# Optimization experiments

Hardware: AMD Instinct MI355X
Metric: run time of the kernel (lower is better)

The kernel has to match this reference:

```python
import jax, jax.numpy as jnp
import numpy as np

N_NODES = 50000
N_EDGES = 800000
IN_DIM = 256
OUT_DIM = 256


def setup_inputs() -> dict:
    key = jax.random.key(0)
    k_feat, k_src, k_dst, k_w0, k_w1, k_b = jax.random.split(key, 6)
    feat = jax.random.normal(k_feat, (N_NODES, IN_DIM), dtype=jnp.float32)
    src = jax.random.randint(k_src, (N_EDGES,), 0, N_NODES, dtype=jnp.int64)
    dst = jax.random.randint(k_dst, (N_EDGES,), 0, N_NODES, dtype=jnp.int64)
    # GraphConv weights (Glorot-ish scale) and biases
    W0 = jax.random.normal(k_w0, (IN_DIM, OUT_DIM), dtype=jnp.float32) / np.sqrt(IN_DIM)
    W1 = jax.random.normal(k_w1, (OUT_DIM, OUT_DIM), dtype=jnp.float32) / np.sqrt(OUT_DIM)
    b0 = jnp.zeros((OUT_DIM,), dtype=jnp.float32)
    b1 = jnp.zeros((OUT_DIM,), dtype=jnp.float32)
    # single shared nn.PReLU parameter (torch default init 0.25)
    prelu_a = jnp.asarray(0.25, dtype=jnp.float32)
    return {"feat": feat, "src": src, "dst": dst,
            "W0": W0, "b0": b0, "W1": W1, "b1": b1, "prelu_a": prelu_a}


def _prelu(x, a):
    return jnp.where(x >= 0, x, a * x)


def reference(feat, src, dst, W0, b0, W1, b1, prelu_a):
    N = feat.shape[0]
    ones = jnp.ones((src.shape[0],), dtype=feat.dtype)
    out_deg = jnp.zeros((N,), dtype=feat.dtype).at[src].add(ones)
    in_deg = jnp.zeros((N,), dtype=feat.dtype).at[dst].add(ones)
    # DGL norm='both': clamp degrees to >=1 before rsqrt
    norm_s = jax.lax.rsqrt(jnp.maximum(out_deg, 1.0))[:, None]  # [N,1]
    norm_d = jax.lax.rsqrt(jnp.maximum(in_deg, 1.0))[:, None]   # [N,1]

    def graph_conv(h, W, b):
        # h' = D_in^{-1/2} A (D_out^{-1/2} h) W + b
        msg = (h * norm_s)[src]                                   # [E, d]
        agg = jax.ops.segment_sum(msg, dst, num_segments=N)       # [N, d]
        return (agg * norm_d) @ W + b

    h = _prelu(graph_conv(feat, W0, b0), prelu_a)
    hg = jnp.sum(h, axis=0, keepdims=True)                        # SumPooling [1, d]
    h = _prelu(graph_conv(h, W1, b1), prelu_a)
    hg = jnp.concatenate([hg, jnp.sum(h, axis=0, keepdims=True)], axis=-1)
    return (h, hg)
```

## Files before the change

### kernel.cpp

```cpp
#include <hip/hip_runtime.h>
#include <stdint.h>

#define NN 50000
#define NE 800000
#define DIM 256

#define HB 128
#define HT 512
#define HALF 25000

#define NSLICE 4
#define SCH 64
#define NPB 64
#define ECH 2048

#define GR 64
#define GB ((NN + GR - 1) / GR)

#define SCB 49

typedef __bf16 bf16x8 __attribute__((ext_vector_type(8)));
typedef float f32x4 __attribute__((ext_vector_type(4)));
typedef float f32x2 __attribute__((ext_vector_type(2)));
typedef unsigned u32x4 __attribute__((ext_vector_type(4)));
typedef int i32x4 __attribute__((ext_vector_type(4)));

__device__ __forceinline__ unsigned short f2bf(float f) {
  union { float f; unsigned u; } v; v.f = f;
  unsigned r = v.u + 0x7fffu + ((v.u >> 16) & 1u);
  return (unsigned short)(r >> 16);
}

__device__ __forceinline__ void gload_lds16(const void* g, void* l) {
  __builtin_amdgcn_global_load_lds(
      (const __attribute__((address_space(1))) unsigned*)g,
      (__attribute__((address_space(3))) unsigned*)l, 16, 0, 0);
}

__global__ __launch_bounds__(HT) void hist_kernel(const int* __restrict__ src,
                                                  const int* __restrict__ dst,
                                                  unsigned* __restrict__ Hs,
                                                  unsigned* __restrict__ Hd) {
  __shared__ unsigned lds[HALF];
  const int tid = threadIdx.x;
  const int phase = blockIdx.x >> 7;
  const int b = blockIdx.x & (HB - 1);
  const int* arr = phase ? dst : src;
  unsigned* H = phase ? Hd : Hs;
  for (int w = tid; w < HALF; w += HT) lds[w] = 0u;
  __syncthreads();
  for (int e = b * HT + tid; e < NE; e += HB * HT) {
    unsigned n = (unsigned)arr[e];
    atomicAdd(&lds[n >> 1], 1u << ((n & 1) * 16));
  }
  __syncthreads();
  for (int w = tid; w < HALF; w += HT)
    H[(size_t)b * HALF + w] = lds[w];
}

__global__ __launch_bounds__(512) void reduce_norm_kernel(const unsigned* __restrict__ Hs,
                                                          const unsigned* __restrict__ Hd,
                                                          unsigned* __restrict__ Pd,
                                                          int* __restrict__ in_cnt,
                                                          float* __restrict__ norm_s,
                                                          float* __restrict__ norm_d,
                                                          float* __restrict__ hg,
                                                          int* __restrict__ csum) {
  __shared__ int ws[8];
  const int tid = threadIdx.x;
  const int w = blockIdx.x * 512 + tid;
  if (blockIdx.x == 0) hg[tid] = 0.f;
  unsigned ss = 0, dd = 0;
  if (w < HALF) {
    for (int b = 0; b < HB; ++b) {
      Pd[(size_t)b * HALF + w] = dd;
      ss += Hs[(size_t)b * HALF + w];
      dd += Hd[(size_t)b * HALF + w];
    }
    int n0 = w * 2;
    unsigned s0 = ss & 0xffffu, s1 = ss >> 16;
    unsigned d0 = dd & 0xffffu, d1 = dd >> 16;
    in_cnt[n0] = (int)d0;
    in_cnt[n0 + 1] = (int)d1;
    norm_s[n0] = rsqrtf(fmaxf((float)s0, 1.0f));
    norm_s[n0 + 1] = rsqrtf(fmaxf((float)s1, 1.0f));
    norm_d[n0] = rsqrtf(fmaxf((float)d0, 1.0f));
    norm_d[n0 + 1] = rsqrtf(fmaxf((float)d1, 1.0f));
  }
  int deg = (int)((dd & 0xffffu) + (dd >> 16));
  int lane = tid & 63, wave = tid >> 6;
#pragma unroll
  for (int off = 32; off; off >>= 1) deg += __shfl_down(deg, off, 64);
  if (lane == 0) ws[wave] = deg;
  __syncthreads();
  if (tid == 0) {
    int s = 0;
#pragma unroll
    for (int i = 0; i < 8; ++i) s += ws[i];
    csum[blockIdx.x] = s;
  }
}

__global__ __launch_bounds__(256) void scan_write_kernel(const int* __restrict__ in_cnt,
                                                         const int* __restrict__ csum,
                                                         int* __restrict__ row_ptr) {
  __shared__ int wsum[4];
  int tid = threadIdx.x, lane = tid & 63, wave = tid >> 6;
  int cv = (lane < SCB) ? csum[lane] : 0;
  int cincl = cv;
#pragma unroll
  for (int off = 1; off < 64; off <<= 1) {
    int t = __shfl_up(cincl, off, 64);
    if (lane >= off) cincl += t;
  }
  int myoff = __shfl(cincl, blockIdx.x, 64) - __shfl(cv, blockIdx.x, 64);
  int total = __shfl(cincl, SCB - 1, 64);
  if (blockIdx.x == 0 && tid == 0) row_ptr[NN] = total;

  int i0 = blockIdx.x * 1024 + tid * 4;
  int v[4];
#pragma unroll
  for (int j = 0; j < 4; ++j) {
    int i = i0 + j;
    v[j] = (i < NN) ? in_cnt[i] : 0;
  }
  int tsum = v[0] + v[1] + v[2] + v[3];
  int incl = tsum;
#pragma unroll
  for (int off = 1; off < 64; off <<= 1) {
    int t = __shfl_up(incl, off, 64);
    if (lane >= off) incl += t;
  }
  if (lane == 63) wsum[wave] = incl;
  __syncthreads();
  int woff = 0;
  for (int w = 0; w < wave; ++w) woff += wsum[w];
  int run = myoff + woff + (incl - tsum);
#pragma unroll
  for (int j = 0; j < 4; ++j) {
    int i = i0 + j;
    if (i < NN) row_ptr[i] = run;
    run += v[j];
  }
}

__global__ __launch_bounds__(HT) void fill_kernel(const int* __restrict__ src,
                                                  const int* __restrict__ dst,
                                                  const int* __restrict__ row_ptr,
                                                  const unsigned* __restrict__ Pd,
                                                  int* __restrict__ colx) {
  __shared__ unsigned lds[HALF];
  const int tid = threadIdx.x;
  const int b = blockIdx.x;
  for (int w = tid; w < HALF; w += HT) lds[w] = 0u;
  __syncthreads();
  for (int e = b * HT + tid; e < NE; e += HB * HT) {
    int n = dst[e];
    int sh = (n & 1) * 16;
    unsigned old = atomicAdd(&lds[n >> 1], 1u << sh);
    unsigned rank = (old >> sh) & 0xffffu;
    unsigned pref = (Pd[(size_t)b * HALF + (n >> 1)] >> sh) & 0xffffu;
    colx[row_ptr[n] + (int)pref + (int)rank] = src[e] << 7;
  }
}

__device__ __forceinline__ void swizzleW_body(const float* __restrict__ W,
                                              unsigned short* __restrict__ Wb, int idx) {
  int lane = idx & 63;
  int blk = idx >> 6;
  int kc = blk & 7, nt = blk >> 3;
  int kbase = kc * 32 + (lane >> 4) * 8;
  int col = nt * 16 + (lane & 15);
  ushort4 o0, o1;
  o0.x = f2bf(W[(size_t)(kbase + 0) * DIM + col]);
  o0.y = f2bf(W[(size_t)(kbase + 1) * DIM + col]);
  o0.z = f2bf(W[(size_t)(kbase + 2) * DIM + col]);
  o0.w = f2bf(W[(size_t)(kbase + 3) * DIM + col]);
  o1.x = f2bf(W[(size_t)(kbase + 4) * DIM + col]);
  o1.y = f2bf(W[(size_t)(kbase + 5) * DIM + col]);
  o1.z = f2bf(W[(size_t)(kbase + 6) * DIM + col]);
  o1.w = f2bf(W[(size_t)(kbase + 7) * DIM + col]);
  ((ushort4*)Wb)[idx * 2 + 0] = o0;
  ((ushort4*)Wb)[idx * 2 + 1] = o1;
}

__global__ void prep_kernel(const float* __restrict__ feat, const float* __restrict__ norm_s,
                            unsigned short* __restrict__ featb,
                            const float* __restrict__ W0, unsigned short* __restrict__ Wb0,
                            const float* __restrict__ W1, unsigned short* __restrict__ Wb1) {
  int blk = blockIdx.x;
  if (blk < 12500) {
    int i = blk * 256 + threadIdx.x;
    int node = i >> 6;
    int ch4 = i & 63;
    float s = norm_s[node];
    float4 v = ((const float4*)feat)[i];
    ushort4 o;
    o.x = f2bf(v.x * s); o.y = f2bf(v.y * s); o.z = f2bf(v.z * s); o.w = f2bf(v.w * s);
    int sl = ch4 >> 4;
    int w4 = ch4 & 15;
    ((ushort4*)featb)[(size_t)sl * (NN * 16) + (size_t)node * 16 + w4] = o;
  } else if (blk < 12532) {
    swizzleW_body(W0, Wb0, (blk - 12500) * 256 + threadIdx.x);
  } else {
    swizzleW_body(W1, Wb1, (blk - 12532) * 256 + threadIdx.x);
  }
}

__device__ __forceinline__ void acc_row(f32x2* a, u32x4 p) {
  f32x2 v0 = { __uint_as_float(p.x << 16), __uint_as_float(p.x & 0xffff0000u) };
  a[0] += v0;
  f32x2 v1 = { __uint_as_float(p.y << 16), __uint_as_float(p.y & 0xffff0000u) };
  a[1] += v1;
  f32x2 v2 = { __uint_as_float(p.z << 16), __uint_as_float(p.z & 0xffff0000u) };
  a[2] += v2;
  f32x2 v3 = { __uint_as_float(p.w << 16), __uint_as_float(p.w & 0xffff0000u) };
  a[3] += v3;
}

__global__ __launch_bounds__(256) void agg_kernel(const unsigned short* __restrict__ X,
                                                  unsigned short* __restrict__ agg,
                                                  const int* __restrict__ row_ptr,
                                                  const int* __restrict__ colx,
                                                  const float* __restrict__ norm_d) {
  __shared__ int ecol[ECH];
  const int s = blockIdx.x & (NSLICE - 1);
  const int nb = blockIdx.x >> 2;
  const int tid = threadIdx.x;
  const int grp = tid >> 3;
  const int cl = tid & 7;

  const int nfirst = nb * NPB;
  const int nlast = (nfirst + NPB < NN) ? (nfirst + NPB) : NN;
  const int estart = row_ptr[nfirst];
  const int eend = row_ptr[nlast];

  const char* Xp = (const char*)(X + (size_t)s * (NN * SCH));
  const int lsub = cl * 16;

  int nodes[2];
  nodes[0] = nfirst + grp;
  nodes[1] = nfirst + 32 + grp;

  f32x2 acc2[2][4];
#pragma unroll
  for (int q = 0; q < 2; ++q)
#pragma unroll
    for (int j = 0; j < 4; ++j) acc2[q][j] = (f32x2){0.f, 0.f};

  int e_[2], end_[2];
#pragma unroll
  for (int q = 0; q < 2; ++q) {
    if (nodes[q] < NN) { e_[q] = row_ptr[nodes[q]]; end_[q] = row_ptr[nodes[q] + 1]; }
    else { e_[q] = 0; end_[q] = 0; }
  }

  const int base0 = estart & ~3;
  for (int base = base0; base < eend; base += ECH) {
    const int lim = (base + ECH < eend) ? (base + ECH) : eend;
    __syncthreads();
    for (int k = base + tid * 4; k < lim; k += 1024) {
      i32x4 v = *(const i32x4*)(colx + k);
      *(i32x4*)&ecol[k - base] = v;
    }
    __syncthreads();
#pragma unroll
    for (int q = 0; q < 2; ++q) {
      int e = e_[q];
      const int hi = (end_[q] < lim) ? end_[q] : lim;
      f32x2* a = acc2[q];
      for (; e + 16 <= hi; e += 16) {
        int o_[16];
#pragma unroll
        for (int j = 0; j < 16; ++j) o_[j] = ecol[e - base + j];
        u32x4 r_[16];
#pragma unroll
        for (int j = 0; j < 16; ++j)
          r_[j] = *(const u32x4*)(Xp + (size_t)(unsigned)(o_[j] | lsub));
#pragma unroll
        for (int j = 0; j < 16; ++j) acc_row(a, r_[j]);
      }
      if (e + 8 <= hi) {
        int o_[8];
#pragma unroll
        for (int j = 0; j < 8; ++j) o_[j] = ecol[e - base + j];
        u32x4 r_[8];
#pragma unroll
        for (int j = 0; j < 8; ++j)
          r_[j] = *(const u32x4*)(Xp + (size_t)(unsigned)(o_[j] | lsub));
#pragma unroll
        for (int j = 0; j < 8; ++j) acc_row(a, r_[j]);
        e += 8;
      }
      if (e + 4 <= hi) {
        int o_[4];
#pragma unroll
        for (int j = 0; j < 4; ++j) o_[j] = ecol[e - base + j];
        u32x4 r_[4];
#pragma unroll
        for (int j = 0; j < 4; ++j)
          r_[j] = *(const u32x4*)(Xp + (size_t)(unsigned)(o_[j] | lsub));
#pragma unroll
        for (int j = 0; j < 4; ++j) acc_row(a, r_[j]);
        e += 4;
      }
      for (; e < hi; ++e) {
        int o0 = ecol[e - base];
        u32x4 r = *(const u32x4*)(Xp + (size_t)(unsigned)(o0 | lsub));
        acc_row(a, r);
      }
      e_[q] = e;
    }
  }

#pragma unroll
  for (int q = 0; q < 2; ++q) {
    int node = nodes[q];
    if (node < NN) {
      float nd = norm_d[node];
      f32x2* a = acc2[q];
      u32x4 o;
      o.x = (unsigned)f2bf(a[0].x * nd) | ((unsigned)f2bf(a[0].y * nd) << 16);
      o.y = (unsigned)f2bf(a[1].x * nd) | ((unsigned)f2bf(a[1].y * nd) << 16);
      o.z = (unsigned)f2bf(a[2].x * nd) | ((unsigned)f2bf(a[2].y * nd) << 16);
      o.w = (unsigned)f2bf(a[3].x * nd) | ((unsigned)f2bf(a[3].y * nd) << 16);
      unsigned pcol = (unsigned)(s * 128 + cl * 16) ^ (((unsigned)node & 7u) << 4);
      __builtin_nontemporal_store(o, (u32x4*)((char*)agg + (size_t)node * 512 + pcol));
    }
  }
}

#define FROW 260
__global__ __launch_bounds__(256) void gemm_mfma_kernel(const unsigned short* __restrict__ A,
                                                        const unsigned short* __restrict__ Wb,
                                                        const float* __restrict__ bias,
                                                        const float* __restrict__ prelu_a_ptr,
                                                        const float* __restrict__ norm_s,
                                                        float* __restrict__ C,
                                                        unsigned short* __restrict__ Cb,
                                                        float* __restrict__ hg_part) {
  __shared__ __attribute__((aligned(16))) char Asb[GR * 512];
  int tid = threadIdx.x;
  int r0 = blockIdx.x * GR;
  const char* Ab = (const char*)A;
#pragma unroll
  for (int p = 0; p < 8; ++p) {
    int off = p * 4096 + tid * 16;
    int row = off >> 9;
    int col = off & 511;
    int grow = r0 + row;
    if (grow > NN - 1) grow = NN - 1;
    gload_lds16(Ab + (size_t)grow * 512 + col, Asb + off);
  }
  __syncthreads();

  int wave = tid >> 6, lane = tid & 63;
  int quad = lane >> 4, l16 = lane & 15;

  f32x4 acc[4][4];
#pragma unroll
  for (int mt = 0; mt < 4; ++mt)
#pragma unroll
    for (int nti = 0; nti < 4; ++nti)
      acc[mt][nti] = (f32x4){0.f, 0.f, 0.f, 0.f};

#pragma unroll
  for (int kc = 0; kc < 8; ++kc) {
    bf16x8 a[4], b[4];
#pragma unroll
    for (int mt = 0; mt < 4; ++mt) {
      int row = mt * 16 + l16;
      int c = (kc * 64 + quad * 16) ^ ((row & 7) << 4);
      a[mt] = *(const bf16x8*)(Asb + row * 512 + c);
    }
#pragma unroll
    for (int nti = 0; nti < 4; ++nti) {
      int nt = wave * 4 + nti;
      b[nti] = *(const bf16x8*)(Wb + ((size_t)(nt * 8 + kc) * 64 + lane) * 8);
    }
#pragma unroll
    for (int mt = 0; mt < 4; ++mt)
#pragma unroll
      for (int nti = 0; nti < 4; ++nti)
        acc[mt][nti] = __builtin_amdgcn_mfma_f32_16x16x32_bf16(a[mt], b[nti], acc[mt][nti], 0, 0, 0);
  }

  float pa = *prelu_a_ptr;
  float bv[4], cs[4];
#pragma unroll
  for (int nti = 0; nti < 4; ++nti) {
    bv[nti] = bias[wave * 64 + nti * 16 + l16];
    cs[nti] = 0.f;
  }
#pragma unroll
  for (int mt = 0; mt < 4; ++mt) {
#pragma unroll
    for (int nti = 0; nti < 4; ++nti) {
#pragma unroll
      for (int r = 0; r < 4; ++r) {
        int rowg = r0 + mt * 16 + quad * 4 + r;
        float x = acc[mt][nti][r] + bv[nti];
        x = (x >= 0.f) ? x : pa * x;
        acc[mt][nti][r] = x;
        if (rowg < NN) cs[nti] += x;
      }
    }
  }
#pragma unroll
  for (int nti = 0; nti < 4; ++nti) {
    cs[nti] += __shfl_xor(cs[nti], 16, 64);
    cs[nti] += __shfl_xor(cs[nti], 32, 64);
  }
  if (quad == 0) {
#pragma unroll
    for (int nti = 0; nti < 4; ++nti)
      hg_part[(size_t)blockIdx.x * 256 + wave * 64 + nti * 16 + l16] = cs[nti];
  }

  float* LF = (float*)Asb;
#pragma unroll
  for (int chunk = 0; chunk < 4; ++chunk) {
    __syncthreads();
#pragma unroll
    for (int nti = 0; nti < 4; ++nti) {
      int colw = wave * 64 + nti * 16 + l16;
#pragma unroll
      for (int r = 0; r < 4; ++r)
        LF[(quad * 4 + r) * FROW + colw] = acc[chunk][nti][r];
    }
    __syncthreads();
    int rowbase = r0 + chunk * 16;
    if (C) {
#pragma unroll
      for (int s = 0; s < 4; ++s) {
        int g = s * 256 + tid;
        int row = g >> 6, cg = g & 63;
        int rowg = rowbase + row;
        if (rowg < NN) {
          float4 v = *(const float4*)&LF[row * FROW + cg * 4];
          *(float4*)(C + (size_t)rowg * DIM + cg * 4) = v;
        }
      }
    }
    if (Cb) {
#pragma unroll
      for (int s = 0; s < 2; ++s) {
        int g = s * 256 + tid;
        int row = g >> 5, cg = g & 31;
        int rowg = rowbase + row;
        if (rowg < NN) {
          float ns = norm_s[rowg];
          float4 v0 = *(const float4*)&LF[row * FROW + cg * 8];
          float4 v1 = *(const float4*)&LF[row * FROW + cg * 8 + 4];
          uint4 o;
          o.x = (unsigned)f2bf(v0.x * ns) | ((unsigned)f2bf(v0.y * ns) << 16);
          o.y = (unsigned)f2bf(v0.z * ns) | ((unsigned)f2bf(v0.w * ns) << 16);
          o.z = (unsigned)f2bf(v1.x * ns) | ((unsigned)f2bf(v1.y * ns) << 16);
          o.w = (unsigned)f2bf(v1.z * ns) | ((unsigned)f2bf(v1.w * ns) << 16);
          unsigned short* outp = Cb + (size_t)(cg >> 3) * (NN * SCH)
                               + (size_t)rowg * SCH + (size_t)(cg & 7) * 8;
          *(uint4*)outp = o;
        }
      }
    }
  }
}

__global__ __launch_bounds__(256) void hg_reduce_kernel(const float* __restrict__ hg_part,
                                                        float* __restrict__ hg) {
  const int layer = blockIdx.x >> 3;
  const int chunk = blockIdx.x & 7;
  const int c = threadIdx.x;
  const float* base = hg_part + (size_t)layer * GB * 256;
  const int per = (GB + 7) / 8;
  int b0 = chunk * per;
  int b1 = (b0 + per < GB) ? (b0 + per) : GB;
  float s0 = 0.f, s1 = 0.f, s2 = 0.f, s3 = 0.f;
  int b = b0;
  for (; b + 4 <= b1; b += 4) {
    s0 += base[(size_t)(b + 0) * 256 + c];
    s1 += base[(size_t)(b + 1) * 256 + c];
    s2 += base[(size_t)(b + 2) * 256 + c];
    s3 += base[(size_t)(b + 3) * 256 + c];
  }
  for (; b < b1; ++b) s0 += base[(size_t)b * 256 + c];
  atomicAdd(&hg[layer * 256 + c], (s0 + s1) + (s2 + s3));
}

extern "C" void kernel_launch(void* const* d_in, const int* in_sizes, int n_in,
                              void* d_out, int out_size, void* d_ws, size_t ws_size,
                              hipStream_t stream) {
  const float* feat = (const float*)d_in[0];
  const int* src    = (const int*)d_in[1];
  const int* dst    = (const int*)d_in[2];
  const float* W0   = (const float*)d_in[3];
  const float* b0   = (const float*)d_in[4];
  const float* W1   = (const float*)d_in[5];
  const float* b1   = (const float*)d_in[6];
  const float* pa   = (const float*)d_in[7];

  float* out_h = (float*)d_out;
  float* hg    = out_h + (size_t)NN * DIM;

  char* w = (char*)d_ws;
  int* in_cnt   = (int*)w;        w += (size_t)NN * 4;
  float* norm_s = (float*)w;      w += (size_t)NN * 4;
  float* norm_d = (float*)w;      w += (size_t)NN * 4;
  int* row_ptr  = (int*)w;        w += (size_t)(NN + 16) * 4;
  int* colx     = (int*)w;        w += (size_t)(NE + 4) * 4;
  int* csum     = (int*)w;        w += 64 * 4;
  unsigned short* Wb0 = (unsigned short*)w;  w += (size_t)DIM * DIM * 2;
  unsigned short* Wb1 = (unsigned short*)w;  w += (size_t)DIM * DIM * 2;
  float* hg_part = (float*)w;     w += (size_t)2 * GB * 256 * 4;
  uintptr_t ap = ((uintptr_t)w + 255) & ~(uintptr_t)255;
  unsigned short* featb = (unsigned short*)ap;
  unsigned short* aggb  = featb + (size_t)NN * DIM;
  unsigned* Hs = (unsigned*)featb;
  unsigned* Hd = Hs + (size_t)HB * HALF;
  unsigned* Pd = (unsigned*)aggb;

  const int agg_blocks = NSLICE * ((NN + NPB - 1) / NPB);

  hist_kernel<<<2 * HB, HT, 0, stream>>>(src, dst, Hs, Hd);
  reduce_norm_kernel<<<SCB, 512, 0, stream>>>(Hs, Hd, Pd, in_cnt, norm_s, norm_d, hg, csum);
  prep_kernel<<<12564, 256, 0, stream>>>(feat, norm_s, featb, W0, Wb0, W1, Wb1);
  scan_write_kernel<<<SCB, 256, 0, stream>>>(in_cnt, csum, row_ptr);
  fill_kernel<<<HB, HT, 0, stream>>>(src, dst, row_ptr, Pd, colx);

  agg_kernel<<<agg_blocks, 256, 0, stream>>>(featb, aggb, row_ptr, colx, norm_d);
  gemm_mfma_kernel<<<GB, 256, 0, stream>>>(aggb, Wb0, b0, pa, norm_s,
                                           (float*)nullptr, featb, hg_part);

  agg_kernel<<<agg_blocks, 256, 0, stream>>>(featb, aggb, row_ptr, colx, norm_d);
  gemm_mfma_kernel<<<GB, 256, 0, stream>>>(aggb, Wb1, b1, pa, norm_s,
                                           out_h, (unsigned short*)nullptr, hg_part + (size_t)GB * 256);

  hg_reduce_kernel<<<16, 256, 0, stream>>>(hg_part, hg);
}
```

Before: 302.1 us.

## Process two row tiles per GEMM block, prefetching the second tile's LDS load

The MFMA GEMM kernel now handles two 64-row tiles per block and issues the global-to-LDS loads for both tiles up front. A partial vmcnt wait lets compute on the first tile start while the second tile is still loading, hiding part of the load latency. The fp32 output store also becomes a nontemporal store. In exchange, LDS per block doubles to 64 KB, which can lower occupancy, and the grid is halved, so fewer blocks are available to spread across the CUs.

```diff
diff --git a/kernel.cpp b/kernel.cpp
--- a/kernel.cpp
+++ b/kernel.cpp
@@ -24,6 +24,7 @@
 typedef float f32x2 __attribute__((ext_vector_type(2)));
 typedef unsigned u32x4 __attribute__((ext_vector_type(4)));
 typedef int i32x4 __attribute__((ext_vector_type(4)));
+typedef float f32x4v __attribute__((ext_vector_type(4)));
 
 __device__ __forceinline__ unsigned short f2bf(float f) {
   union { float f; unsigned u; } v; v.f = f;
@@ -339,130 +340,142 @@
                                                         float* __restrict__ C,
                                                         unsigned short* __restrict__ Cb,
                                                         float* __restrict__ hg_part) {
-  __shared__ __attribute__((aligned(16))) char Asb[GR * 512];
+  __shared__ __attribute__((aligned(16))) char Asb[2][GR * 512];
   int tid = threadIdx.x;
-  int r0 = blockIdx.x * GR;
   const char* Ab = (const char*)A;
-#pragma unroll
-  for (int p = 0; p < 8; ++p) {
-    int off = p * 4096 + tid * 16;
-    int row = off >> 9;
-    int col = off & 511;
-    int grow = r0 + row;
-    if (grow > NN - 1) grow = NN - 1;
-    gload_lds16(Ab + (size_t)grow * 512 + col, Asb + off);
-  }
-  __syncthreads();
+
+#pragma unroll
+  for (int h = 0; h < 2; ++h) {
+    int r0h = (blockIdx.x * 2 + h) * GR;
+#pragma unroll
+    for (int p = 0; p < 8; ++p) {
+      int off = p * 4096 + tid * 16;
+      int row = off >> 9;
+      int col = off & 511;
+      int grow = r0h + row;
+      if (grow > NN - 1) grow = NN - 1;
+      gload_lds16(Ab + (size_t)grow * 512 + col, &Asb[h][off]);
+    }
+  }
+  asm volatile("s_waitcnt vmcnt(8)" ::: "memory");
+  __builtin_amdgcn_s_barrier();
 
   int wave = tid >> 6, lane = tid & 63;
   int quad = lane >> 4, l16 = lane & 15;
-
-  f32x4 acc[4][4];
-#pragma unroll
-  for (int mt = 0; mt < 4; ++mt)
-#pragma unroll
-    for (int nti = 0; nti < 4; ++nti)
-      acc[mt][nti] = (f32x4){0.f, 0.f, 0.f, 0.f};
-
-#pragma unroll
-  for (int kc = 0; kc < 8; ++kc) {
-    bf16x8 a[4], b[4];
+  float pa = *prelu_a_ptr;
+  float bv[4];
+#pragma unroll
+  for (int nti = 0; nti < 4; ++nti)
+    bv[nti] = bias[wave * 64 + nti * 16 + l16];
+
+  for (int h = 0; h < 2; ++h) {
+    const char* As = Asb[h];
+    int r0 = (blockIdx.x * 2 + h) * GR;
+
+    f32x4 acc[4][4];
+#pragma unroll
+    for (int mt = 0; mt < 4; ++mt)
+#pragma unroll
+      for (int nti = 0; nti < 4; ++nti)
+        acc[mt][nti] = (f32x4){0.f, 0.f, 0.f, 0.f};
+
+#pragma unroll
+    for (int kc = 0; kc < 8; ++kc) {
+      bf16x8 a[4], b[4];
+#pragma unroll
+      for (int mt = 0; mt < 4; ++mt) {
+        int row = mt * 16 + l16;
+        int c = (kc * 64 + quad * 16) ^ ((row & 7) << 4);
+        a[mt] = *(const bf16x8*)(As + row * 512 + c);
+      }
+#pragma unroll
+      for (int nti = 0; nti < 4; ++nti) {
+        int nt = wave * 4 + nti;
+        b[nti] = *(const bf16x8*)(Wb + ((size_t)(nt * 8 + kc) * 64 + lane) * 8);
+      }
+#pragma unroll
+      for (int mt = 0; mt < 4; ++mt)
+#pragma unroll
+        for (int nti = 0; nti < 4; ++nti)
+          acc[mt][nti] = __builtin_amdgcn_mfma_f32_16x16x32_bf16(a[mt], b[nti], acc[mt][nti], 0, 0, 0);
+    }
+
+    float cs[4];
+#pragma unroll
+    for (int nti = 0; nti < 4; ++nti) cs[nti] = 0.f;
 #pragma unroll
     for (int mt = 0; mt < 4; ++mt) {
-      int row = mt * 16 + l16;
-      int c = (kc * 64 + quad * 16) ^ ((row & 7) << 4);
-      a[mt] = *(const bf16x8*)(Asb + row * 512 + c);
+#pragma unroll
+      for (int nti = 0; nti < 4; ++nti) {
+#pragma unroll
+        for (int r = 0; r < 4; ++r) {
+          int rowg = r0 + mt * 16 + quad * 4 + r;
+          float x = acc[mt][nti][r] + bv[nti];
+          x = (x >= 0.f) ? x : pa * x;
+          acc[mt][nti][r] = x;
+          if (rowg < NN) cs[nti] += x;
+        }
+      }
     }
 #pragma unroll
     for (int nti = 0; nti < 4; ++nti) {
-      int nt = wave * 4 + nti;
-      b[nti] = *(const bf16x8*)(Wb + ((size_t)(nt * 8 + kc) * 64 + lane) * 8);
-    }
-#pragma unroll
-    for (int mt = 0; mt < 4; ++mt)
+      cs[nti] += __shfl_xor(cs[nti], 16, 64);
+      cs[nti] += __shfl_xor(cs[nti], 32, 64);
+    }
+    if (quad == 0) {
 #pragma unroll
       for (int nti = 0; nti < 4; ++nti)
-        acc[mt][nti] = __builtin_amdgcn_mfma_f32_16x16x32_bf16(a[mt], b[nti], acc[mt][nti], 0, 0, 0);
-  }
-
-  float pa = *prelu_a_ptr;
-  float bv[4], cs[4];
-#pragma unroll
-  for (int nti = 0; nti < 4; ++nti) {
-    bv[nti] = bias[wave * 64 + nti * 16 + l16];
-    cs[nti] = 0.f;
-  }
-#pragma unroll
-  for (int mt = 0; mt < 4; ++mt) {
-#pragma unroll
-    for (int nti = 0; nti < 4; ++nti) {
-#pragma unroll
-      for (int r = 0; r < 4; ++r) {
-        int rowg = r0 + mt * 16 + quad * 4 + r;
-        float x = acc[mt][nti][r] + bv[nti];
-        x = (x >= 0.f) ? x : pa * x;
-        acc[mt][nti][r] = x;
-        if (rowg < NN) cs[nti] += x;
-      }
-    }
-  }
-#pragma unroll
-  for (int nti = 0; nti < 4; ++nti) {
-    cs[nti] += __shfl_xor(cs[nti], 16, 64);
-    cs[nti] += __shfl_xor(cs[nti], 32, 64);
-  }
-  if (quad == 0) {
-#pragma unroll
-    for (int nti = 0; nti < 4; ++nti)
-      hg_part[(size_t)blockIdx.x * 256 + wave * 64 + nti * 16 + l16] = cs[nti];
-  }
-
-  float* LF = (float*)Asb;
-#pragma unroll
-  for (int chunk = 0; chunk < 4; ++chunk) {
-    __syncthreads();
-#pragma unroll
-    for (int nti = 0; nti < 4; ++nti) {
-      int colw = wave * 64 + nti * 16 + l16;
-#pragma unroll
-      for (int r = 0; r < 4; ++r)
-        LF[(quad * 4 + r) * FROW + colw] = acc[chunk][nti][r];
-    }
-    __syncthreads();
-    int rowbase = r0 + chunk * 16;
-    if (C) {
-#pragma unroll
-      for (int s = 0; s < 4; ++s) {
-        int g = s * 256 + tid;
-        int row = g >> 6, cg = g & 63;
-        int rowg = rowbase + row;
-        if (rowg < NN) {
-          float4 v = *(const float4*)&LF[row * FROW + cg * 4];
-          *(float4*)(C + (size_t)rowg * DIM + cg * 4) = v;
+        hg_part[(size_t)(blockIdx.x * 2 + h) * 256 + wave * 64 + nti * 16 + l16] = cs[nti];
+    }
+
+    float* LF = (float*)Asb[h];
+#pragma unroll
+    for (int chunk = 0; chunk < 4; ++chunk) {
+      __syncthreads();
+#pragma unroll
+      for (int nti = 0; nti < 4; ++nti) {
+        int colw = wave * 64 + nti * 16 + l16;
+#pragma unroll
+        for (int r = 0; r < 4; ++r)
+          LF[(quad * 4 + r) * FROW + colw] = acc[chunk][nti][r];
+      }
+      __syncthreads();
+      int rowbase = r0 + chunk * 16;
+      if (C) {
+#pragma unroll
+        for (int s = 0; s < 4; ++s) {
+          int g = s * 256 + tid;
+          int row = g >> 6, cg = g & 63;
+          int rowg = rowbase + row;
+          if (rowg < NN) {
+            f32x4v v = *(const f32x4v*)&LF[row * FROW + cg * 4];
+            __builtin_nontemporal_store(v, (f32x4v*)(C + (size_t)rowg * DIM + cg * 4));
+          }
         }
       }
-    }
-    if (Cb) {
-#pragma unroll
-      for (int s = 0; s < 2; ++s) {
-        int g = s * 256 + tid;
-        int row = g >> 5, cg = g & 31;
-        int rowg = rowbase + row;
-        if (rowg < NN) {
-          float ns = norm_s[rowg];
-          float4 v0 = *(const float4*)&LF[row * FROW + cg * 8];
-          float4 v1 = *(const float4*)&LF[row * FROW + cg * 8 + 4];
-          uint4 o;
-          o.x = (unsigned)f2bf(v0.x * ns) | ((unsigned)f2bf(v0.y * ns) << 16);
-          o.y = (unsigned)f2bf(v0.z * ns) | ((unsigned)f2bf(v0.w * ns) << 16);
-          o.z = (unsigned)f2bf(v1.x * ns) | ((unsigned)f2bf(v1.y * ns) << 16);
-          o.w = (unsigned)f2bf(v1.z * ns) | ((unsigned)f2bf(v1.w * ns) << 16);
-          unsigned short* outp = Cb + (size_t)(cg >> 3) * (NN * SCH)
-                               + (size_t)rowg * SCH + (size_t)(cg & 7) * 8;
-          *(uint4*)outp = o;
+      if (Cb) {
+#pragma unroll
+        for (int s = 0; s < 2; ++s) {
+          int g = s * 256 + tid;
+          int row = g >> 5, cg = g & 31;
+          int rowg = rowbase + row;
+          if (rowg < NN) {
+            float ns = norm_s[rowg];
+            float4 v0 = *(const float4*)&LF[row * FROW + cg * 8];
+            float4 v1 = *(const float4*)&LF[row * FROW + cg * 8 + 4];
+            uint4 o;
+            o.x = (unsigned)f2bf(v0.x * ns) | ((unsigned)f2bf(v0.y * ns) << 16);
+            o.y = (unsigned)f2bf(v0.z * ns) | ((unsigned)f2bf(v0.w * ns) << 16);
+            o.z = (unsigned)f2bf(v1.x * ns) | ((unsigned)f2bf(v1.y * ns) << 16);
+            o.w = (unsigned)f2bf(v1.z * ns) | ((unsigned)f2bf(v1.w * ns) << 16);
+            unsigned short* outp = Cb + (size_t)(cg >> 3) * (NN * SCH)
+                                 + (size_t)rowg * SCH + (size_t)(cg & 7) * 8;
+            *(uint4*)outp = o;
+          }
         }
       }
     }
+    if (h == 0) __syncthreads();
   }
 }
 
@@ -520,6 +533,7 @@
   unsigned* Pd = (unsigned*)aggb;
 
   const int agg_blocks = NSLICE * ((NN + NPB - 1) / NPB);
+  const int gemm_blocks = GB / 2;
 
   hist_kernel<<<2 * HB, HT, 0, stream>>>(src, dst, Hs, Hd);
   reduce_norm_kernel<<<SCB, 512, 0, stream>>>(Hs, Hd, Pd, in_cnt, norm_s, norm_d, hg, csum);
@@ -528,12 +542,12 @@
   fill_kernel<<<HB, HT, 0, stream>>>(src, dst, row_ptr, Pd, colx);
 
   agg_kernel<<<agg_blocks, 256, 0, stream>>>(featb, aggb, row_ptr, colx, norm_d);
-  gemm_mfma_kernel<<<GB, 256, 0, stream>>>(aggb, Wb0, b0, pa, norm_s,
-                                           (float*)nullptr, featb, hg_part);
+  gemm_mfma_kernel<<<gemm_blocks, 256, 0, stream>>>(aggb, Wb0, b0, pa, norm_s,
+                                                    (float*)nullptr, featb, hg_part);
 
   agg_kernel<<<agg_blocks, 256, 0, stream>>>(featb, aggb, row_ptr, colx, norm_d);
-  gemm_mfma_kernel<<<GB, 256, 0, stream>>>(aggb, Wb1, b1, pa, norm_s,
-                                           out_h, (unsigned short*)nullptr, hg_part + (size_t)GB * 256);
+  gemm_mfma_kernel<<<gemm_blocks, 256, 0, stream>>>(aggb, Wb1, b1, pa, norm_s,
+                                                    out_h, (unsigned short*)nullptr, hg_part + (size_t)GB * 256);
 
   hg_reduce_kernel<<<16, 256, 0, stream>>>(hg_part, hg);
 }
```

After: 308.3 us. 1.02x slower.
